# Performance work log

Hardware: AMD Instinct MI355X
Metric: run time of the kernel (lower is better)

The kernel has to match this reference:

```python
import jax, jax.numpy as jnp
import numpy as np

I_SIZE = 8      # interval_size
WS = 8          # window_size
SHIFT = 4       # window_size // 2
HG = 4          # grid-attn heads (num_heads // 2)
HS = 4          # swin/window heads (num_heads // 2)


def cln(x, g, b, eps=1e-5):
    # channel LayerNorm over axis 1 of NCHW
    mu = x.mean(axis=1, keepdims=True)
    var = ((x - mu) ** 2).mean(axis=1, keepdims=True)
    return (x - mu) / jnp.sqrt(var + eps) * g[None, :, None, None] + b[None, :, None, None]


def conv1x1(x, w, b):
    return jnp.einsum('bchw,oc->bohw', x, w) + b[None, :, None, None]


def grid_shuffle(x, I):
    B, C, H, W = x.shape
    H1, W1 = H // I, W // I
    x = x.reshape(B, C, H1, I, W1, I).transpose(0, 3, 5, 1, 2, 4)
    return x.reshape(B * I * I, C, H1, W1)


def grid_unshuffle(x, I):
    Bi, C, H1, W1 = x.shape
    B = Bi // (I * I)
    x = x.reshape(B, I, I, C, H1, W1).transpose(0, 3, 4, 1, 5, 2)
    return x.reshape(B, C, H1 * I, W1 * I)


def rel_pos_index(wh, ww):
    coords = np.stack(np.meshgrid(np.arange(wh), np.arange(ww), indexing='ij')).reshape(2, -1)
    rel = (coords[:, :, None] - coords[:, None, :]).transpose(1, 2, 0)
    rel[:, :, 0] += wh - 1
    rel[:, :, 1] += ww - 1
    rel[:, :, 0] *= 2 * ww - 1
    return rel.sum(-1)  # (N, N) int


def dyn_pos_bias(H1, W1, w1, b1, w2, b2, w3, b3):
    # dynamic position bias MLP: (2,) relative coords -> heads
    ch = np.arange(1 - H1, H1, dtype=np.float32)
    cw = np.arange(1 - W1, W1, dtype=np.float32)
    rel = np.stack(np.meshgrid(ch, cw, indexing='ij'), axis=-1).reshape(-1, 2)
    t = jnp.asarray(rel)
    t = jax.nn.relu(t @ w1.T + b1)
    t = jax.nn.relu(t @ w2.T + b2)
    t = t @ w3.T + b3  # ((2H1-1)*(2W1-1), heads)
    idx = rel_pos_index(H1, W1)
    return t[idx].transpose(2, 0, 1)[None]  # (1, heads, N, N)


def mha2d(q, k, v, bias, heads, pw, pb):
    B, C, H, W = q.shape
    hd, N = C // heads, H * W
    sp = lambda t: t.reshape(B, heads, hd, N).transpose(0, 1, 3, 2)
    qh, kh, vh = sp(q), sp(k), sp(v)
    attn = jax.nn.softmax(jnp.einsum('bhnd,bhmd->bhnm', qh * hd ** -0.5, kh) + bias, axis=-1)
    out = jnp.einsum('bhnm,bhmd->bhnd', attn, vh).transpose(0, 1, 3, 2).reshape(B, C, H, W)
    return conv1x1(out, pw, pb)


def swin_mask(H, W, ws, shift):
    img = np.zeros((H, W), np.float32)
    cnt = 0
    for hs in (slice(0, H - ws), slice(H - ws, H - shift), slice(H - shift, H)):
        for wsl in (slice(0, W - ws), slice(W - ws, W - shift), slice(W - shift, W)):
            img[hs, wsl] = cnt
            cnt += 1
    mw = img.reshape(H // ws, ws, W // ws, ws).transpose(0, 2, 1, 3).reshape(-1, ws * ws)
    m = mw[:, None, :] - mw[:, :, None]
    return jnp.asarray(np.where(m != 0, -100.0, 0.0).astype(np.float32))  # (nW, N, N)


def swin_attn(x, qkv_w, qkv_b, rpb, pw, pb, ws, shift, heads):
    B, C, H, W = x.shape
    hd, N = C // heads, ws * ws
    if shift > 0:
        x = jnp.roll(x, (-shift, -shift), axis=(2, 3))
    nh, nw = H // ws, W // ws
    nW = nh * nw
    xw = x.reshape(B, C, nh, ws, nw, ws).transpose(0, 2, 4, 3, 5, 1).reshape(B * nW, N, C)
    qkv = (xw @ qkv_w.T + qkv_b).reshape(B * nW, N, 3, heads, hd).transpose(2, 0, 3, 1, 4)
    q, k, v = qkv[0], qkv[1], qkv[2]
    attn = jnp.einsum('bhnd,bhmd->bhnm', q * hd ** -0.5, k)
    attn = attn + rpb[rel_pos_index(ws, ws)].transpose(2, 0, 1)[None]
    if shift > 0:
        mask = swin_mask(H, W, ws, shift)
        attn = (attn.reshape(B, nW, heads, N, N) + mask[None, :, None]).reshape(B * nW, heads, N, N)
    attn = jax.nn.softmax(attn, axis=-1)
    out = jnp.einsum('bhnm,bhmd->bhnd', attn, v).transpose(0, 2, 1, 3).reshape(B * nW, N, C)
    out = out @ pw.T + pb
    out = out.reshape(B, nh, nw, ws, ws, C).transpose(0, 5, 1, 3, 2, 4).reshape(B, C, H, W)
    if shift > 0:
        out = jnp.roll(out, (shift, shift), axis=(2, 3))
    return out


def setup_inputs() -> dict:
    ks = iter(jax.random.split(jax.random.key(0), 64))
    w = lambda *s: jax.random.normal(next(ks), s, jnp.float32) * 0.02
    d, dg, ds, hid = 128, 64, 32, 256
    return dict(
        x=jax.random.normal(next(ks), (4, d, 128, 128), jnp.float32),
        ln_g=jnp.ones(d), ln_b=jnp.zeros(d),
        ga_qkv_w=w(3 * dg, dg), ga_qkv_b=jnp.zeros(3 * dg),
        ga_gp_w=w(dg, dg), ga_gp_b=jnp.zeros(dg),
        pos_w1=w(16, 2), pos_b1=jnp.zeros(16),
        pos_w2=w(16, 16), pos_b2=jnp.zeros(16),
        pos_w3=w(HG, 16), pos_b3=jnp.zeros(HG),
        a1_pw=w(dg, dg), a1_pb=jnp.zeros(dg),
        a2_pw=w(dg, dg), a2_pb=jnp.zeros(dg),
        sw_qkv_w=w(3 * ds, ds), sw_qkv_b=jnp.zeros(3 * ds),
        sw_rpb=w((2 * WS - 1) ** 2, HS), sw_pw=w(ds, ds), sw_pb=jnp.zeros(ds),
        wn_qkv_w=w(3 * ds, ds), wn_qkv_b=jnp.zeros(3 * ds),
        wn_rpb=w((2 * WS - 1) ** 2, HS), wn_pw=w(ds, ds), wn_pb=jnp.zeros(ds),
        fc_w=w(d, d), fc_b=jnp.zeros(d),
        n2_g=jnp.ones(d), n2_b=jnp.zeros(d),
        m1_w=w(hid, d), m1_b=jnp.zeros(hid),
        m2_w=w(d, hid), m2_b=jnp.zeros(d),
    )


def reference(x, ln_g, ln_b, ga_qkv_w, ga_qkv_b, ga_gp_w, ga_gp_b,
              pos_w1, pos_b1, pos_w2, pos_b2, pos_w3, pos_b3,
              a1_pw, a1_pb, a2_pw, a2_pb,
              sw_qkv_w, sw_qkv_b, sw_rpb, sw_pw, sw_pb,
              wn_qkv_w, wn_qkv_b, wn_rpb, wn_pw, wn_pb,
              fc_w, fc_b, n2_g, n2_b, m1_w, m1_b, m2_w, m2_b):
    B, C, H, W = x.shape
    shortcut = x
    xg, xs, xw = jnp.split(x, [C // 2, C // 2 + C // 4], axis=1)

    # --- grid attention branch (C/2 channels) ---
    qkv = conv1x1(xg, ga_qkv_w, ga_qkv_b)
    x_grid = conv1x1(grid_shuffle(xg, I_SIZE), ga_gp_w, ga_gp_b)
    qkv = grid_shuffle(qkv, I_SIZE)
    H1, W1 = H // I_SIZE, W // I_SIZE
    pbias = dyn_pos_bias(H1, W1, pos_w1, pos_b1, pos_w2, pos_b2, pos_w3, pos_b3)
    q, k, v = jnp.split(qkv, 3, axis=1)
    t = mha2d(x_grid, k, v, pbias, HG, a1_pw, a1_pb)
    t = mha2d(q, x_grid, t, pbias, HG, a2_pw, a2_pb)
    xg_attn = grid_unshuffle(t, I_SIZE)

    # --- shifted / plain window attention branches (C/4 each) ---
    xs_attn = swin_attn(xs, sw_qkv_w, sw_qkv_b, sw_rpb, sw_pw, sw_pb, WS, SHIFT, HS)
    xw_attn = swin_attn(xw, wn_qkv_w, wn_qkv_b, wn_rpb, wn_pw, wn_pb, WS, 0, HS)

    x = jnp.concatenate([xw_attn, xs_attn, xg_attn], axis=1)
    x = cln(conv1x1(x, fc_w, fc_b), ln_g, ln_b)
    x = shortcut + x
    h = conv1x1(x, m1_w, m1_b)
    h = jax.nn.gelu(h, approximate=False)
    h = conv1x1(h, m2_w, m2_b)
    return x + cln(h, n2_g, n2_b) + shortcut
```

## Files before the change

kernel.cpp:

```cpp
#include <hip/hip_runtime.h>
#include <hip/hip_bf16.h>
#include <cstdint>


typedef __attribute__((ext_vector_type(8))) short bf8_t;
typedef __attribute__((ext_vector_type(4))) float f4_t;

__device__ __forceinline__ float bf2f(unsigned short u) {
  union { unsigned int i; float f; } x; x.i = ((unsigned int)u) << 16; return x.f;
}
__device__ __forceinline__ unsigned short f2bf(float f) {
  union { float f; unsigned int i; } x; x.f = f;
  unsigned int r = x.i + 0x7FFFu + ((x.i >> 16) & 1u);
  return (unsigned short)(r >> 16);
}
__device__ __forceinline__ unsigned int pk2(float a, float b) {
  unsigned int d;
  asm("v_cvt_pk_bf16_f32 %0, %1, %2" : "=v"(d) : "v"(a), "v"(b));
  return d;
}

#define MB (1048576L)

__global__ void setup_k(
    const float* __restrict__ w0, const float* __restrict__ w1,
    const float* __restrict__ w2, const float* __restrict__ w3,
    const float* __restrict__ w4, const float* __restrict__ w5,
    const float* __restrict__ w6,
    const float* __restrict__ qkv_b, const float* __restrict__ gp_b,
    const float* __restrict__ sw_w, const float* __restrict__ sw_b,
    const float* __restrict__ wn_w, const float* __restrict__ wn_b,
    const float* __restrict__ sw_rpb, const float* __restrict__ wn_rpb,
    const float* __restrict__ pw1, const float* __restrict__ pb1,
    const float* __restrict__ pw2, const float* __restrict__ pb2,
    const float* __restrict__ pw3, const float* __restrict__ pb3,
    unsigned short* __restrict__ wbf, float* __restrict__ biasQG,
    unsigned short* __restrict__ wq2, float* __restrict__ b192,
    float* __restrict__ rpbT_sw, float* __restrict__ rpbT_wn,
    float* __restrict__ ptab) {
  const float QS = 0.35355339059327373f;
  int t = blockIdx.x * 256 + threadIdx.x;
  if (t < 106496) {
    const float* src; int off; float sc = 1.0f;
    if (t < 12288)      { src = w0; off = 0; }
    else if (t < 16384) { src = w1; off = 12288; sc = 0.25f; }
    else if (t < 20480) { src = w2; off = 16384; }
    else if (t < 24576) { src = w3; off = 20480; }
    else if (t < 40960) { src = w4; off = 24576; }
    else if (t < 73728) { src = w5; off = 40960; }
    else                { src = w6; off = 73728; }
    wbf[t] = f2bf(src[t - off] * sc);
  } else if (t < 106752) {
    int i = t - 106496;
    biasQG[i] = i < 192 ? qkv_b[i] : gp_b[i - 192] * 0.25f;
  } else if (t < 119040) {
    int i = t - 106752;
    int row = i >> 6, col = i & 63;
    float v = 0.0f;
    if (row < 96) { if (col < 32) v = sw_w[row * 32 + col]; }
    else          { if (col >= 32) v = wn_w[(row - 96) * 32 + col - 32]; }
    if ((row % 96) < 32) v *= QS;
    wq2[i] = f2bf(v);
  } else if (t < 119232) {
    int i = t - 119040;
    float v = i < 96 ? sw_b[i] : wn_b[i - 96];
    if ((i % 96) < 32) v *= QS;
    b192[i] = v;
  } else if (t < 152000) {
    int i = t - 119232;
    const float* rpb = i < 16384 ? sw_rpb : wn_rpb;
    float* dst = i < 16384 ? rpbT_sw : rpbT_wn;
    int j = i & 16383;
    int h = j >> 12, r = j & 4095, m = r >> 6, n = r & 63;
    int idx = ((n >> 3) - (m >> 3) + 7) * 15 + ((n & 7) - (m & 7) + 7);
    dst[j] = rpb[idx * 4 + h];
  } else if (t < 152961) {
    int j = t - 152000;
    float chv = (float)(j / 31) - 15.0f;
    float cwv = (float)(j % 31) - 15.0f;
    float t1[16], t2[16];
#pragma unroll
    for (int i = 0; i < 16; ++i) {
      float s = fmaf(pw1[i * 2], chv, fmaf(pw1[i * 2 + 1], cwv, pb1[i]));
      t1[i] = fmaxf(s, 0.0f);
    }
#pragma unroll
    for (int i = 0; i < 16; ++i) {
      float s = pb2[i];
#pragma unroll
      for (int k = 0; k < 16; ++k) s = fmaf(pw2[i * 16 + k], t1[k], s);
      t2[i] = fmaxf(s, 0.0f);
    }
#pragma unroll
    for (int hh = 0; hh < 4; ++hh) {
      float s = pb3[hh];
#pragma unroll
      for (int k = 0; k < 16; ++k) s = fmaf(pw3[hh * 16 + k], t2[k], s);
      ptab[j * 4 + hh] = s;
    }
  }
}

__global__ void pbq_k(const float* __restrict__ table, unsigned short* __restrict__ pbTq) {
  int t = blockIdx.x * 256 + threadIdx.x;
  int h = t >> 16;
  int r = t & 65535;
  int q = r >> 8;
  int m = r & 255;
  int idx = ((q >> 4) - (m >> 4) + 15) * 31 + ((q & 15) - (m & 15) + 15);
  pbTq[t] = f2bf(table[idx * 4 + h]);
}

__global__ __launch_bounds__(256) void tin_k(const float* __restrict__ x,
                                             unsigned short* __restrict__ xTb) {
  __shared__ float tile[64][132];
  const int b = blockIdx.z, px0 = blockIdx.x * 64, tid = threadIdx.x;
#pragma unroll
  for (int i = 0; i < 8; ++i) {
    int e = i * 256 + tid;
    int c = e >> 4, p4 = (e & 15) * 4;
    float4 v = *(const float4*)(x + (((size_t)(b * 128 + c)) << 14) + px0 + p4);
    tile[p4][c] = v.x; tile[p4 + 1][c] = v.y; tile[p4 + 2][c] = v.z; tile[p4 + 3][c] = v.w;
  }
  __syncthreads();
#pragma unroll
  for (int i = 0; i < 8; ++i) {
    int e = i * 256 + tid;
    int px = e >> 5, c4 = (e & 31) * 4;
    uint2 w = {pk2(tile[px][c4], tile[px][c4 + 1]), pk2(tile[px][c4 + 2], tile[px][c4 + 3])};
    *(uint2*)(xTb + ((size_t)(b * 16384 + px0 + px)) * 128 + c4) = w;
  }
}

template <int NF, int KC, int EPI, int OSHUF>
__global__ __launch_bounds__(256) void gemm_k(
    const unsigned short* __restrict__ A, int a_rs, int a_c0,
    const unsigned short* __restrict__ W, const float* __restrict__ bias,
    const float* __restrict__ g, const float* __restrict__ bb,
    const unsigned short* __restrict__ resf, const unsigned short* __restrict__ resb,
    void* __restrict__ out, int o_rs, int o_c0) {
  __shared__ __align__(16) char Asw[128 * 128];
  __shared__ __align__(16) char Bsw[NF * 16 * 128];
  const int tid = threadIdx.x;
  const int lane = tid & 63, wv = tid >> 6, wpx = wv * 32;
  const int lr = lane & 15, lg = lane >> 4;
  const int px0 = blockIdx.x * 128;
  const int co0 = blockIdx.y * (NF * 16);

  f4_t acc[2][NF];
#pragma unroll
  for (int mf = 0; mf < 2; ++mf)
#pragma unroll
    for (int nf = 0; nf < NF; ++nf) acc[mf][nf] = (f4_t){0.f, 0.f, 0.f, 0.f};

  for (int kc = 0; kc < KC; ++kc) {
    const int k0 = kc * 64;
    if (kc) __syncthreads();
#pragma unroll
    for (int i = 0; i < 4; ++i) {
      int e = i * 256 + tid;
      int row = e >> 3, q8 = e & 7;
      const unsigned short* src = A + (size_t)(px0 + row) * a_rs + a_c0 + k0 + q8 * 8;
      *(uint4*)(Asw + row * 128 + ((q8 ^ (row & 7)) << 4)) = *(const uint4*)src;
    }
#pragma unroll
    for (int i = 0; i < NF / 2; ++i) {
      int e = i * 256 + tid;
      int row = e >> 3, q8 = e & 7;
      const unsigned short* src = W + (size_t)(co0 + row) * (KC * 64) + k0 + q8 * 8;
      *(uint4*)(Bsw + row * 128 + ((q8 ^ (row & 7)) << 4)) = *(const uint4*)src;
    }
    __syncthreads();
#pragma unroll
    for (int ks = 0; ks < 2; ++ks) {
      const int xk = (((ks * 4) + lg) ^ (lane & 7)) << 4;
      bf8_t av[2], bv[NF];
#pragma unroll
      for (int mf = 0; mf < 2; ++mf)
        av[mf] = *(const bf8_t*)(Asw + (wpx + mf * 16 + lr) * 128 + xk);
#pragma unroll
      for (int nf = 0; nf < NF; ++nf)
        bv[nf] = *(const bf8_t*)(Bsw + (nf * 16 + lr) * 128 + xk);
#pragma unroll
      for (int mf = 0; mf < 2; ++mf)
#pragma unroll
        for (int nf = 0; nf < NF; ++nf)
          acc[mf][nf] = __builtin_amdgcn_mfma_f32_16x16x32_bf16(av[mf], bv[nf], acc[mf][nf], 0, 0, 0);
    }
  }

  float bco[NF];
#pragma unroll
  for (int nf = 0; nf < NF; ++nf) bco[nf] = bias[co0 + nf * 16 + lr];

  if constexpr (EPI >= 2) {
    float gv[NF], bbv[NF];
#pragma unroll
    for (int nf = 0; nf < NF; ++nf) { gv[nf] = g[nf * 16 + lr]; bbv[nf] = bb[nf * 16 + lr]; }
#pragma unroll
    for (int mf = 0; mf < 2; ++mf)
#pragma unroll
      for (int nf = 0; nf < NF; ++nf)
#pragma unroll
        for (int r = 0; r < 4; ++r) acc[mf][nf][r] += bco[nf];
#pragma unroll
    for (int mf = 0; mf < 2; ++mf) {
      float mus[4], rss[4];
#pragma unroll
      for (int r = 0; r < 4; ++r) {
        float s = 0.f, q = 0.f;
#pragma unroll
        for (int nf = 0; nf < NF; ++nf) {
          float v = acc[mf][nf][r];
          s += v; q += v * v;
        }
#pragma unroll
        for (int msk = 1; msk < 16; msk <<= 1) {
          s += __shfl_xor(s, msk);
          q += __shfl_xor(q, msk);
        }
        float mu = s * (1.0f / 128.0f);
        float var = q * (1.0f / 128.0f) - mu * mu;
        mus[r] = mu;
        rss[r] = rsqrtf(var + 1e-5f);
      }
      if constexpr (EPI == 2) {
#pragma unroll
        for (int r = 0; r < 4; ++r) {
          int px_e = px0 + wpx + mf * 16 + lg * 4 + r;
          const unsigned short* xr = resf + (size_t)px_e * 128 + lr;
          unsigned short* op = (unsigned short*)out + (size_t)px_e * o_rs + lr;
#pragma unroll
          for (int nf = 0; nf < NF; ++nf) {
            float v = (acc[mf][nf][r] - mus[r]) * rss[r] * gv[nf] + bbv[nf] + bf2f(xr[nf * 16]);
            op[nf * 16] = f2bf(v);
          }
        }
      } else {
        int pxb = px0 + wpx + mf * 16 + lg * 4;
        int b_ = pxb >> 14, p_ = pxb & 16383;
#pragma unroll
        for (int nf = 0; nf < NF; ++nf) {
          int ch = lr + nf * 16;
          float vr[4];
#pragma unroll
          for (int r = 0; r < 4; ++r) {
            float xv  = bf2f(resf[(size_t)(pxb + r) * 128 + ch]);
            float x2v = bf2f(resb[(size_t)(pxb + r) * 128 + ch]);
            vr[r] = (acc[mf][nf][r] - mus[r]) * rss[r] * gv[nf] + bbv[nf] + xv + x2v;
          }
          float4 v4 = {vr[0], vr[1], vr[2], vr[3]};
          *(float4*)((float*)out + (((size_t)(b_ * 128 + ch)) << 14) + p_) = v4;
        }
      }
    }
  } else {
#pragma unroll
    for (int mf = 0; mf < 2; ++mf) {
#pragma unroll
      for (int r = 0; r < 4; ++r) {
        int px_e = px0 + wpx + mf * 16 + lg * 4 + r;
        size_t orow;
        int cadj = co0;
        if constexpr (OSHUF == 0) {
          orow = (size_t)px_e;
        } else if constexpr (OSHUF == 1) {
          int b = px_e >> 14, p = px_e & 16383, hh = p >> 7, w_ = p & 127;
          orow = (size_t)(b * 64 + (hh & 7) * 8 + (w_ & 7)) * 256 + ((hh >> 3) * 16 + (w_ >> 3));
        } else if constexpr (OSHUF == 2) {
          int gbb = px_e >> 8, n = px_e & 255;
          int b = gbb >> 6, ih = (gbb >> 3) & 7, iw = gbb & 7;
          orow = (size_t)b * 16384 + ((n >> 4) * 8 + ih) * 128 + (n & 15) * 8 + iw;
        } else {
          int brx = (co0 >= 96);
          int b = px_e >> 14, p = px_e & 16383, hh = p >> 7, w_ = p & 127;
          int sh = brx ? 0 : 4;
          int h2 = (hh - sh) & 127, w2_ = (w_ - sh) & 127;
          orow = (size_t)brx * 65536 + (size_t)b * 16384 +
                 (size_t)(((h2 >> 3) * 16 + (w2_ >> 3)) * 64 + (h2 & 7) * 8 + (w2_ & 7));
          cadj = co0 - brx * 96;
        }
        unsigned short* op = (unsigned short*)out + orow * o_rs + o_c0 + cadj + lr;
#pragma unroll
        for (int nf = 0; nf < NF; ++nf) {
          float v = acc[mf][nf][r] + bco[nf];
          if constexpr (EPI == 1) v = 0.5f * v * (1.0f + erff(v * 0.7071067811865475f));
          op[nf * 16] = f2bf(v);
        }
      }
    }
  }
}

__global__ __launch_bounds__(256) void gattn_k(
    const unsigned short* __restrict__ Q, int q_rs, int q_c0,
    const unsigned short* __restrict__ K, int k_rs, int k_c0,
    const unsigned short* __restrict__ V, int v_rs, int v_c0,
    const unsigned short* __restrict__ pbTq, unsigned short* __restrict__ outb,
    int o_rs, int o_c0) {
  __shared__ __align__(16) unsigned short K_lds[256 * 16];
  __shared__ __align__(16) unsigned short Vt[16 * 256];
  __shared__ __align__(16) unsigned short P_lds[4 * 64 * 32];
  const int gb = blockIdx.x, h = blockIdx.y, tid = threadIdx.x;
  const int lane = tid & 63, wv = tid >> 6;
  const int lr = lane & 15, lg = lane >> 4;
  const int q0 = wv * 64;

  {
    const unsigned short* kp = K + (size_t)(gb * 256 + tid) * k_rs + k_c0 + h * 16;
    *(uint4*)&K_lds[tid * 16]     = *(const uint4*)kp;
    *(uint4*)&K_lds[tid * 16 + 8] = *(const uint4*)(kp + 8);
    const unsigned short* vp = V + (size_t)(gb * 256 + tid) * v_rs + v_c0 + h * 16;
    uint4 va = *(const uint4*)vp;
    uint4 vb = *(const uint4*)(vp + 8);
    unsigned int w8[8] = {va.x, va.y, va.z, va.w, vb.x, vb.y, vb.z, vb.w};
    int chb = (tid >> 3);
    int wi = tid & 7;
#pragma unroll
    for (int w = 0; w < 8; ++w) {
      int d0 = 2 * w, d1 = 2 * w + 1;
      Vt[d0 * 256 + ((chb ^ (d0 & 7)) << 3) + wi] = (unsigned short)(w8[w] & 0xffff);
      Vt[d1 * 256 + ((chb ^ (d1 & 7)) << 3) + wi] = (unsigned short)(w8[w] >> 16);
    }
  }
  bf8_t bq[4];
  const bf8_t bz = {0, 0, 0, 0, 0, 0, 0, 0};
#pragma unroll
  for (int qt = 0; qt < 4; ++qt) {
    bq[qt] = bz;
    if (lg < 2)
      bq[qt] = *(const bf8_t*)(Q + (size_t)(gb * 256 + q0 + qt * 16 + lr) * q_rs + q_c0 + h * 16 + lg * 8);
  }
  __syncthreads();

  const f4_t z4 = {0.f, 0.f, 0.f, 0.f};
  f4_t oacc[4];
  float lrun[4];
#pragma unroll
  for (int qt = 0; qt < 4; ++qt) { oacc[qt] = z4; lrun[qt] = 0.0f; }

  unsigned short* Pw = &P_lds[wv * 64 * 32];

  for (int m0 = 0; m0 < 256; m0 += 32) {
    bf8_t ak0 = bz, ak1 = bz;
    if (lg < 2) {
      ak0 = *(const bf8_t*)&K_lds[(m0 + lr) * 16 + lg * 8];
      ak1 = *(const bf8_t*)&K_lds[(m0 + 16 + lr) * 16 + lg * 8];
    }
    bf8_t av = *(const bf8_t*)&Vt[lr * 256 + ((((m0 >> 3) + lg) ^ (lr & 7)) << 3)];

#pragma unroll
    for (int qt = 0; qt < 4; ++qt) {
      const unsigned short* bq_ =
          pbTq + (((size_t)(h * 256 + q0 + qt * 16 + lr)) << 8) + m0 + lg * 4;
      uint2 u0 = *(const uint2*)bq_;
      uint2 u1 = *(const uint2*)(bq_ + 16);
      f4_t c0v = {bf2f((unsigned short)u0.x), bf2f((unsigned short)(u0.x >> 16)),
                  bf2f((unsigned short)u0.y), bf2f((unsigned short)(u0.y >> 16))};
      f4_t c1v = {bf2f((unsigned short)u1.x), bf2f((unsigned short)(u1.x >> 16)),
                  bf2f((unsigned short)u1.y), bf2f((unsigned short)(u1.y >> 16))};
      f4_t st0 = __builtin_amdgcn_mfma_f32_16x16x32_bf16(ak0, bq[qt], c0v, 0, 0, 0);
      f4_t st1 = __builtin_amdgcn_mfma_f32_16x16x32_bf16(ak1, bq[qt], c1v, 0, 0, 0);
      float p0[4], p1[4], ls = 0.0f;
#pragma unroll
      for (int r = 0; r < 4; ++r) {
        p0[r] = __expf(st0[r]);
        p1[r] = __expf(st1[r]);
        ls += p0[r] + p1[r];
      }
      ls += __shfl_xor(ls, 16);
      ls += __shfl_xor(ls, 32);
      lrun[qt] += ls;
      int row = qt * 16 + lr;
      int rw3 = row & 3;
      uint2 w0 = {pk2(p0[0], p0[1]), pk2(p0[2], p0[3])};
      uint2 w1 = {pk2(p1[0], p1[1]), pk2(p1[2], p1[3])};
      *(uint2*)&Pw[row * 32 + ((((lg >> 1)) ^ rw3) << 3) + (lg & 1) * 4]     = w0;
      *(uint2*)&Pw[row * 32 + (((2 + (lg >> 1)) ^ rw3) << 3) + (lg & 1) * 4] = w1;
    }
#pragma unroll
    for (int qt = 0; qt < 4; ++qt) {
      int row = qt * 16 + lr;
      bf8_t bp = *(const bf8_t*)&Pw[row * 32 + ((lg ^ (row & 3)) << 3)];
      oacc[qt] = __builtin_amdgcn_mfma_f32_16x16x32_bf16(av, bp, oacc[qt], 0, 0, 0);
    }
  }

#pragma unroll
  for (int qt = 0; qt < 4; ++qt) {
    float inv = 1.0f / lrun[qt];
    uint2 o;
    o.x = pk2(oacc[qt][0] * inv, oacc[qt][1] * inv);
    o.y = pk2(oacc[qt][2] * inv, oacc[qt][3] * inv);
    unsigned short* op = outb + (size_t)(gb * 256 + q0 + qt * 16 + lr) * o_rs + o_c0 + h * 16 + lg * 4;
    *(uint2*)op = o;
  }
}

__global__ __launch_bounds__(256) void swat_k(
    const unsigned short* __restrict__ qkv2,
    const float* __restrict__ rpbT_sw, const float* __restrict__ rpbT_wn,
    const float* __restrict__ sw_pw, const float* __restrict__ sw_pb,
    const float* __restrict__ wn_pw, const float* __restrict__ wn_pb,
    unsigned short* __restrict__ yT) {
  __shared__ __align__(16) unsigned short Vt[4 * 8 * 64];
  __shared__ __align__(16) unsigned short Pt[4 * 64 * 64];
  __shared__ __align__(16) unsigned short aoT[4 * 64 * 32];
  const int tid = threadIdx.x, lane = tid & 63, wv = tid >> 6;
  const int lr = lane & 15, lg = lane >> 4;
  const int br = blockIdx.y;
  const int win = blockIdx.x * 4 + wv;
  const int b = win >> 8, wl = win & 255, wh = wl >> 4, ww = wl & 15;
  const float* rpbT = br ? rpbT_wn : rpbT_sw;
  const float* pw   = br ? wn_pw : sw_pw;
  const float* pb   = br ? wn_pb : sw_pb;
  const int shift = br ? 0 : 4;
  const int yc0 = br ? 0 : 32;
  const bool edge = (shift > 0) && (wh == 15 || ww == 15);

  const unsigned short* qw = qkv2 + (size_t)br * 65536 * 96 + (size_t)win * 64 * 96;
  const f4_t z4 = {0.f, 0.f, 0.f, 0.f};
  const bf8_t bz = {0, 0, 0, 0, 0, 0, 0, 0};
  unsigned short* Vw = &Vt[wv * 8 * 64];
  unsigned short* Pw = &Pt[wv * 64 * 64];
  unsigned short* aw_ = &aoT[wv * 64 * 32];

#pragma unroll 1
  for (int h = 0; h < 4; ++h) {
    {
      uint4 v = *(const uint4*)(qw + lane * 96 + 64 + h * 8);
      unsigned int w4[4] = {v.x, v.y, v.z, v.w};
      int chb = lane >> 3, wi = lane & 7;
#pragma unroll
      for (int j = 0; j < 4; ++j) {
        int d0 = 2 * j, d1 = 2 * j + 1;
        Vw[d0 * 64 + ((chb ^ (d0 & 7)) << 3) + wi] = (unsigned short)(w4[j] & 0xffff);
        Vw[d1 * 64 + ((chb ^ (d1 & 7)) << 3) + wi] = (unsigned short)(w4[j] >> 16);
      }
    }
    bf8_t bq[4];
#pragma unroll
    for (int nt = 0; nt < 4; ++nt) {
      bq[nt] = bz;
      if (lg == 0) bq[nt] = *(const bf8_t*)(qw + (nt * 16 + lr) * 96 + h * 8);
    }
    f4_t st[4][4];
#pragma unroll
    for (int mt = 0; mt < 4; ++mt) {
      bf8_t ak = bz;
      if (lg == 0) ak = *(const bf8_t*)(qw + (mt * 16 + lr) * 96 + 32 + h * 8);
#pragma unroll
      for (int nt = 0; nt < 4; ++nt) {
        const float* rp = rpbT + h * 4096 + (mt * 16 + lg * 4) * 64 + nt * 16 + lr;
        f4_t cb = {rp[0], rp[64], rp[128], rp[192]};
        st[mt][nt] = __builtin_amdgcn_mfma_f32_16x16x32_bf16(ak, bq[nt], cb, 0, 0, 0);
      }
    }
#pragma unroll
    for (int nt = 0; nt < 4; ++nt) {
      float sv[16];
#pragma unroll
      for (int mt = 0; mt < 4; ++mt)
#pragma unroll
        for (int r = 0; r < 4; ++r) sv[mt * 4 + r] = st[mt][nt][r];
      if (edge) {
        int n = nt * 16 + lr;
        int regn = ((wh < 15) ? 0 : (((n >> 3) < 4) ? 1 : 2)) * 3 +
                   ((ww < 15) ? 0 : (((n & 7) < 4) ? 1 : 2));
#pragma unroll
        for (int mt = 0; mt < 4; ++mt)
#pragma unroll
          for (int r = 0; r < 4; ++r) {
            int m = mt * 16 + lg * 4 + r;
            int regm = ((wh < 15) ? 0 : (((m >> 3) < 4) ? 1 : 2)) * 3 +
                       ((ww < 15) ? 0 : (((m & 7) < 4) ? 1 : 2));
            if (regm != regn) sv[mt * 4 + r] -= 100.0f;
          }
      }
      float l = 0.0f;
#pragma unroll
      for (int i = 0; i < 16; ++i) {
        sv[i] = __expf(sv[i]);
        l += sv[i];
      }
      l += __shfl_xor(l, 16);
      l += __shfl_xor(l, 32);
      float inv = 1.0f / l;
      int row = nt * 16 + lr, rw7 = lr & 7;
#pragma unroll
      for (int mt = 0; mt < 4; ++mt) {
        uint2 w = {pk2(sv[mt * 4] * inv, sv[mt * 4 + 1] * inv),
                   pk2(sv[mt * 4 + 2] * inv, sv[mt * 4 + 3] * inv)};
        *(uint2*)&Pw[row * 64 + (((2 * mt + (lg >> 1)) ^ rw7) << 3) + (lg & 1) * 4] = w;
      }
    }
    f4_t oa[4] = {z4, z4, z4, z4};
#pragma unroll
    for (int ks = 0; ks < 2; ++ks) {
      bf8_t av = bz;
      if (lr < 8) av = *(const bf8_t*)&Vw[lr * 64 + (((4 * ks + lg) ^ (lr & 7)) << 3)];
#pragma unroll
      for (int nt = 0; nt < 4; ++nt) {
        int row = nt * 16 + lr;
        bf8_t bp = *(const bf8_t*)&Pw[row * 64 + (((4 * ks + lg) ^ (lr & 7)) << 3)];
        oa[nt] = __builtin_amdgcn_mfma_f32_16x16x32_bf16(av, bp, oa[nt], 0, 0, 0);
      }
    }
    if (lg < 2) {
#pragma unroll
      for (int nt = 0; nt < 4; ++nt) {
        uint2 w = {pk2(oa[nt][0], oa[nt][1]), pk2(oa[nt][2], oa[nt][3])};
        int row = nt * 16 + lr;
        *(uint2*)&aw_[row * 32 + ((h ^ (lr & 3)) << 3) + lg * 4] = w;
      }
    }
  }

#pragma unroll
  for (int mt = 0; mt < 2; ++mt) {
    const float* wr = pw + (mt * 16 + lr) * 32 + lg * 8;
    float4 a0 = *(const float4*)wr, a1 = *(const float4*)(wr + 4);
    union { uint4 u; bf8_t v; } aw;
    aw.u.x = pk2(a0.x, a0.y); aw.u.y = pk2(a0.z, a0.w);
    aw.u.z = pk2(a1.x, a1.y); aw.u.w = pk2(a1.z, a1.w);
    float pb0 = pb[mt * 16 + lg * 4], pb1 = pb[mt * 16 + lg * 4 + 1];
    float pb2 = pb[mt * 16 + lg * 4 + 2], pb3 = pb[mt * 16 + lg * 4 + 3];
#pragma unroll
    for (int nt = 0; nt < 4; ++nt) {
      int row = nt * 16 + lr;
      bf8_t bo = *(const bf8_t*)&aw_[row * 32 + ((lg ^ (lr & 3)) << 3)];
      f4_t po = __builtin_amdgcn_mfma_f32_16x16x32_bf16(aw.v, bo, z4, 0, 0, 0);
      int n = nt * 16 + lr;
      int hdst = (wh * 8 + (n >> 3) + shift) & 127;
      int wdst = (ww * 8 + (n & 7) + shift) & 127;
      uint2 w = {pk2(po[0] + pb0, po[1] + pb1), pk2(po[2] + pb2, po[3] + pb3)};
      *(uint2*)(yT + ((size_t)(b * 16384 + hdst * 128 + wdst)) * 128 + yc0 + mt * 16 + lg * 4) = w;
    }
  }
}

extern "C" void kernel_launch(void* const* d_in, const int* in_sizes, int n_in,
                              void* d_out, int out_size, void* d_ws, size_t ws_size,
                              hipStream_t stream) {
  (void)in_sizes; (void)n_in; (void)out_size; (void)ws_size;
  const float* x        = (const float*)d_in[0];
  const float* ln_g     = (const float*)d_in[1];
  const float* ln_b     = (const float*)d_in[2];
  const float* ga_qkv_w = (const float*)d_in[3];
  const float* ga_qkv_b = (const float*)d_in[4];
  const float* ga_gp_w  = (const float*)d_in[5];
  const float* ga_gp_b  = (const float*)d_in[6];
  const float* pos_w1   = (const float*)d_in[7];
  const float* pos_b1   = (const float*)d_in[8];
  const float* pos_w2   = (const float*)d_in[9];
  const float* pos_b2   = (const float*)d_in[10];
  const float* pos_w3   = (const float*)d_in[11];
  const float* pos_b3   = (const float*)d_in[12];
  const float* a1_pw    = (const float*)d_in[13];
  const float* a1_pb    = (const float*)d_in[14];
  const float* a2_pw    = (const float*)d_in[15];
  const float* a2_pb    = (const float*)d_in[16];
  const float* sw_qkv_w = (const float*)d_in[17];
  const float* sw_qkv_b = (const float*)d_in[18];
  const float* sw_rpb   = (const float*)d_in[19];
  const float* sw_pw    = (const float*)d_in[20];
  const float* sw_pb    = (const float*)d_in[21];
  const float* wn_qkv_w = (const float*)d_in[22];
  const float* wn_qkv_b = (const float*)d_in[23];
  const float* wn_rpb   = (const float*)d_in[24];
  const float* wn_pw    = (const float*)d_in[25];
  const float* wn_pb    = (const float*)d_in[26];
  const float* fc_w     = (const float*)d_in[27];
  const float* fc_b     = (const float*)d_in[28];
  const float* n2_g     = (const float*)d_in[29];
  const float* n2_b     = (const float*)d_in[30];
  const float* m1_w     = (const float*)d_in[31];
  const float* m1_b     = (const float*)d_in[32];
  const float* m2_w     = (const float*)d_in[33];
  const float* m2_b     = (const float*)d_in[34];
  float* out = (float*)d_out;
  char* base = (char*)d_ws;

  unsigned short* xTb    = (unsigned short*)(base);
  unsigned short* qgT    = (unsigned short*)(base + 16 * MB);
  unsigned short* t1T    = (unsigned short*)(base + 48 * MB);
  unsigned short* t1pT   = (unsigned short*)(base + 56 * MB);
  unsigned short* yT     = (unsigned short*)(base + 64 * MB);
  unsigned short* x2T    = (unsigned short*)(base + 80 * MB);
  unsigned short* qkv2   = (unsigned short*)(base + 16 * MB);
  unsigned short* hT     = (unsigned short*)(base + 16 * MB);
  unsigned short* pbTq   = (unsigned short*)(base + 96 * MB);
  float*          ptab   = (float*)(base + 97 * MB);
  float*          rpbT_sw= (float*)(base + 97 * MB + 65536);
  float*          rpbT_wn= (float*)(base + 97 * MB + 131072);
  unsigned short* wq2bf  = (unsigned short*)(base + 97 * MB + 196608);
  float*          bias192= (float*)(base + 97 * MB + 229376);
  float*          biasQG = (float*)(base + 97 * MB + 230400);
  unsigned short* wbf    = (unsigned short*)(base + 97 * MB + 262144);

  setup_k<<<598, 256, 0, stream>>>(
      ga_qkv_w, ga_gp_w, a1_pw, a2_pw, fc_w, m1_w, m2_w,
      ga_qkv_b, ga_gp_b,
      sw_qkv_w, sw_qkv_b, wn_qkv_w, wn_qkv_b,
      sw_rpb, wn_rpb,
      pos_w1, pos_b1, pos_w2, pos_b2, pos_w3, pos_b3,
      wbf, biasQG, wq2bf, bias192, rpbT_sw, rpbT_wn, ptab);
  pbq_k<<<1024, 256, 0, stream>>>(ptab, pbTq);

  tin_k<<<dim3(256, 1, 4), 256, 0, stream>>>(x, xTb);

  gemm_k<4, 1, 0, 1><<<dim3(512, 4, 1), 256, 0, stream>>>(
      xTb, 128, 0, wbf, biasQG, nullptr, nullptr, nullptr, nullptr, qgT, 256, 0);

  gattn_k<<<dim3(256, 4), 256, 0, stream>>>(
      qgT, 256, 192, qgT, 256, 64, qgT, 256, 128, pbTq, t1T, 64, 0);
  gemm_k<4, 1, 0, 0><<<dim3(512, 1, 1), 256, 0, stream>>>(
      t1T, 64, 0, wbf + 16384, a1_pb, nullptr, nullptr, nullptr, nullptr, t1pT, 64, 0);

  gattn_k<<<dim3(256, 4), 256, 0, stream>>>(
      qgT, 256, 0, qgT, 256, 192, t1pT, 64, 0, pbTq, t1T, 64, 0);
  gemm_k<4, 1, 0, 2><<<dim3(512, 1, 1), 256, 0, stream>>>(
      t1T, 64, 0, wbf + 20480, a2_pb, nullptr, nullptr, nullptr, nullptr, yT, 128, 64);

  gemm_k<6, 1, 0, 3><<<dim3(512, 2, 1), 256, 0, stream>>>(
      xTb, 128, 64, wq2bf, bias192, nullptr, nullptr, nullptr, nullptr, qkv2, 96, 0);
  swat_k<<<dim3(256, 2), 256, 0, stream>>>(
      qkv2, rpbT_sw, rpbT_wn, sw_pw, sw_pb, wn_pw, wn_pb, yT);

  gemm_k<8, 2, 2, 0><<<dim3(512, 1, 1), 256, 0, stream>>>(
      yT, 128, 0, wbf + 24576, fc_b, ln_g, ln_b, xTb, nullptr, x2T, 128, 0);

  gemm_k<8, 2, 1, 0><<<dim3(512, 2, 1), 256, 0, stream>>>(
      x2T, 128, 0, wbf + 40960, m1_b, nullptr, nullptr, nullptr, nullptr, hT, 256, 0);
  gemm_k<8, 4, 3, 0><<<dim3(512, 1, 1), 256, 0, stream>>>(
      hT, 256, 0, wbf + 73728, m2_b, n2_g, n2_b, xTb, x2T, out, 128, 0);
}
```

Before: 206.5 us.

## Double gattn waves per block and store position bias as transposed fp32

Grid attention blocks now run 8 waves of 32 query rows each instead of 4 waves of 64. The K and V staging is split across the two halves of the block. The position-bias table is stored as fp32 transposed (m-major) rather than bf16 q-major, so each lane reads scalar floats strided by 256 with no conversion step. The aim is more latency hiding and occupancy, at the cost of doubling bias table bytes and using uncoalesced-looking scalar loads for the bias.

```diff
diff --git a/kernel.cpp b/kernel.cpp
--- a/kernel.cpp
+++ b/kernel.cpp
@@ -101,14 +101,14 @@
   }
 }
 
-__global__ void pbq_k(const float* __restrict__ table, unsigned short* __restrict__ pbTq) {
+__global__ void pbT_k(const float* __restrict__ table, float* __restrict__ pbT) {
   int t = blockIdx.x * 256 + threadIdx.x;
-  int h = t >> 16;
+  int hh = t >> 16;
   int r = t & 65535;
-  int q = r >> 8;
-  int m = r & 255;
+  int m = r >> 8;
+  int q = r & 255;
   int idx = ((q >> 4) - (m >> 4) + 15) * 31 + ((q & 15) - (m & 15) + 15);
-  pbTq[t] = f2bf(table[idx * 4 + h]);
+  pbT[t] = table[idx * 4 + hh];
 }
 
 __global__ __launch_bounds__(256) void tin_k(const float* __restrict__ x,
@@ -292,30 +292,31 @@
   }
 }
 
-__global__ __launch_bounds__(256) void gattn_k(
+__global__ __launch_bounds__(512, 8) void gattn_k(
     const unsigned short* __restrict__ Q, int q_rs, int q_c0,
     const unsigned short* __restrict__ K, int k_rs, int k_c0,
     const unsigned short* __restrict__ V, int v_rs, int v_c0,
-    const unsigned short* __restrict__ pbTq, unsigned short* __restrict__ outb,
+    const float* __restrict__ pbT, unsigned short* __restrict__ outb,
     int o_rs, int o_c0) {
   __shared__ __align__(16) unsigned short K_lds[256 * 16];
   __shared__ __align__(16) unsigned short Vt[16 * 256];
-  __shared__ __align__(16) unsigned short P_lds[4 * 64 * 32];
+  __shared__ __align__(16) unsigned short P_lds[8 * 32 * 32];
   const int gb = blockIdx.x, h = blockIdx.y, tid = threadIdx.x;
   const int lane = tid & 63, wv = tid >> 6;
   const int lr = lane & 15, lg = lane >> 4;
-  const int q0 = wv * 64;
-
-  {
+  const int q0 = wv * 32;
+
+  if (tid < 256) {
     const unsigned short* kp = K + (size_t)(gb * 256 + tid) * k_rs + k_c0 + h * 16;
     *(uint4*)&K_lds[tid * 16]     = *(const uint4*)kp;
     *(uint4*)&K_lds[tid * 16 + 8] = *(const uint4*)(kp + 8);
-    const unsigned short* vp = V + (size_t)(gb * 256 + tid) * v_rs + v_c0 + h * 16;
+  } else {
+    int m = tid - 256;
+    const unsigned short* vp = V + (size_t)(gb * 256 + m) * v_rs + v_c0 + h * 16;
     uint4 va = *(const uint4*)vp;
     uint4 vb = *(const uint4*)(vp + 8);
     unsigned int w8[8] = {va.x, va.y, va.z, va.w, vb.x, vb.y, vb.z, vb.w};
-    int chb = (tid >> 3);
-    int wi = tid & 7;
+    int chb = m >> 3, wi = m & 7;
 #pragma unroll
     for (int w = 0; w < 8; ++w) {
       int d0 = 2 * w, d1 = 2 * w + 1;
@@ -323,10 +324,10 @@
       Vt[d1 * 256 + ((chb ^ (d1 & 7)) << 3) + wi] = (unsigned short)(w8[w] >> 16);
     }
   }
-  bf8_t bq[4];
+  bf8_t bq[2];
   const bf8_t bz = {0, 0, 0, 0, 0, 0, 0, 0};
 #pragma unroll
-  for (int qt = 0; qt < 4; ++qt) {
+  for (int qt = 0; qt < 2; ++qt) {
     bq[qt] = bz;
     if (lg < 2)
       bq[qt] = *(const bf8_t*)(Q + (size_t)(gb * 256 + q0 + qt * 16 + lr) * q_rs + q_c0 + h * 16 + lg * 8);
@@ -334,12 +335,12 @@
   __syncthreads();
 
   const f4_t z4 = {0.f, 0.f, 0.f, 0.f};
-  f4_t oacc[4];
-  float lrun[4];
-#pragma unroll
-  for (int qt = 0; qt < 4; ++qt) { oacc[qt] = z4; lrun[qt] = 0.0f; }
-
-  unsigned short* Pw = &P_lds[wv * 64 * 32];
+  f4_t oacc[2];
+  float lrun[2];
+#pragma unroll
+  for (int qt = 0; qt < 2; ++qt) { oacc[qt] = z4; lrun[qt] = 0.0f; }
+
+  unsigned short* Pw = &P_lds[wv * 32 * 32];
 
   for (int m0 = 0; m0 < 256; m0 += 32) {
     bf8_t ak0 = bz, ak1 = bz;
@@ -350,15 +351,10 @@
     bf8_t av = *(const bf8_t*)&Vt[lr * 256 + ((((m0 >> 3) + lg) ^ (lr & 7)) << 3)];
 
 #pragma unroll
-    for (int qt = 0; qt < 4; ++qt) {
-      const unsigned short* bq_ =
-          pbTq + (((size_t)(h * 256 + q0 + qt * 16 + lr)) << 8) + m0 + lg * 4;
-      uint2 u0 = *(const uint2*)bq_;
-      uint2 u1 = *(const uint2*)(bq_ + 16);
-      f4_t c0v = {bf2f((unsigned short)u0.x), bf2f((unsigned short)(u0.x >> 16)),
-                  bf2f((unsigned short)u0.y), bf2f((unsigned short)(u0.y >> 16))};
-      f4_t c1v = {bf2f((unsigned short)u1.x), bf2f((unsigned short)(u1.x >> 16)),
-                  bf2f((unsigned short)u1.y), bf2f((unsigned short)(u1.y >> 16))};
+    for (int qt = 0; qt < 2; ++qt) {
+      const float* bpm = pbT + ((size_t)(h * 256 + m0 + lg * 4) << 8) + q0 + qt * 16 + lr;
+      f4_t c0v = {bpm[0], bpm[256], bpm[512], bpm[768]};
+      f4_t c1v = {bpm[4096], bpm[4352], bpm[4608], bpm[4864]};
       f4_t st0 = __builtin_amdgcn_mfma_f32_16x16x32_bf16(ak0, bq[qt], c0v, 0, 0, 0);
       f4_t st1 = __builtin_amdgcn_mfma_f32_16x16x32_bf16(ak1, bq[qt], c1v, 0, 0, 0);
       float p0[4], p1[4], ls = 0.0f;
@@ -379,7 +375,7 @@
       *(uint2*)&Pw[row * 32 + (((2 + (lg >> 1)) ^ rw3) << 3) + (lg & 1) * 4] = w1;
     }
 #pragma unroll
-    for (int qt = 0; qt < 4; ++qt) {
+    for (int qt = 0; qt < 2; ++qt) {
       int row = qt * 16 + lr;
       bf8_t bp = *(const bf8_t*)&Pw[row * 32 + ((lg ^ (row & 3)) << 3)];
       oacc[qt] = __builtin_amdgcn_mfma_f32_16x16x32_bf16(av, bp, oacc[qt], 0, 0, 0);
@@ -387,7 +383,7 @@
   }
 
 #pragma unroll
-  for (int qt = 0; qt < 4; ++qt) {
+  for (int qt = 0; qt < 2; ++qt) {
     float inv = 1.0f / lrun[qt];
     uint2 o;
     o.x = pk2(oacc[qt][0] * inv, oacc[qt][1] * inv);
@@ -589,7 +585,7 @@
   unsigned short* x2T    = (unsigned short*)(base + 80 * MB);
   unsigned short* qkv2   = (unsigned short*)(base + 16 * MB);
   unsigned short* hT     = (unsigned short*)(base + 16 * MB);
-  unsigned short* pbTq   = (unsigned short*)(base + 96 * MB);
+  float*          pbT    = (float*)(base + 96 * MB);
   float*          ptab   = (float*)(base + 97 * MB);
   float*          rpbT_sw= (float*)(base + 97 * MB + 65536);
   float*          rpbT_wn= (float*)(base + 97 * MB + 131072);
@@ -605,20 +601,20 @@
       sw_rpb, wn_rpb,
       pos_w1, pos_b1, pos_w2, pos_b2, pos_w3, pos_b3,
       wbf, biasQG, wq2bf, bias192, rpbT_sw, rpbT_wn, ptab);
-  pbq_k<<<1024, 256, 0, stream>>>(ptab, pbTq);
+  pbT_k<<<1024, 256, 0, stream>>>(ptab, pbT);
 
   tin_k<<<dim3(256, 1, 4), 256, 0, stream>>>(x, xTb);
 
   gemm_k<4, 1, 0, 1><<<dim3(512, 4, 1), 256, 0, stream>>>(
       xTb, 128, 0, wbf, biasQG, nullptr, nullptr, nullptr, nullptr, qgT, 256, 0);
 
-  gattn_k<<<dim3(256, 4), 256, 0, stream>>>(
-      qgT, 256, 192, qgT, 256, 64, qgT, 256, 128, pbTq, t1T, 64, 0);
+  gattn_k<<<dim3(256, 4), 512, 0, stream>>>(
+      qgT, 256, 192, qgT, 256, 64, qgT, 256, 128, pbT, t1T, 64, 0);
   gemm_k<4, 1, 0, 0><<<dim3(512, 1, 1), 256, 0, stream>>>(
       t1T, 64, 0, wbf + 16384, a1_pb, nullptr, nullptr, nullptr, nullptr, t1pT, 64, 0);
 
-  gattn_k<<<dim3(256, 4), 256, 0, stream>>>(
-      qgT, 256, 0, qgT, 256, 192, t1pT, 64, 0, pbTq, t1T, 64, 0);
+  gattn_k<<<dim3(256, 4), 512, 0, stream>>>(
+      qgT, 256, 0, qgT, 256, 192, t1pT, 64, 0, pbT, t1T, 64, 0);
   gemm_k<4, 1, 0, 2><<<dim3(512, 1, 1), 256, 0, stream>>>(
       t1T, 64, 0, wbf + 20480, a2_pb, nullptr, nullptr, nullptr, nullptr, yT, 128, 64);
 
```

New measurement: 204.5 us. No clear change (-0.9%).
